# Kernel tuning notes

Measured on AMD Instinct MI355X. Metric: run time of the kernel, lower is better.

The kernel has to match this reference:

```python
import jax, jax.numpy as jnp
import numpy as np

NUM_HEADS = 6

def setup_inputs() -> dict:
    key = jax.random.key(0)
    k1, k2, k3 = jax.random.split(key, 3)
    B, N, C = 8, 4096, 768
    x = jax.random.normal(k1, (B, N, C), dtype=jnp.float32)
    # torch Linear weights, stored here as (in, out) so y = x @ w
    w_qkv = jax.random.normal(k2, (C, 3 * C), dtype=jnp.float32) * (C ** -0.5)
    w_proj = jax.random.normal(k3, (C, C), dtype=jnp.float32) * (C ** -0.5)
    b_proj = jnp.zeros((C,), dtype=jnp.float32)
    return {"x": x, "w_qkv": w_qkv, "w_proj": w_proj, "b_proj": b_proj}

def reference(x, w_qkv, w_proj, b_proj):
    B, N, C = x.shape
    H = NUM_HEADS
    D = C // H
    scale = D ** -0.5
    qkv = (x @ w_qkv).reshape(B, N, 3, H, D)
    q, k, v = qkv[:, :, 0], qkv[:, :, 1], qkv[:, :, 2]  # each (B, N, H, D)
    # NOTE: faithful to source — no permute, so attention is over the HEAD axis
    attn = jnp.einsum('bnhd,bngd->bnhg', q, k) * scale  # (B, N, H, H)
    attn = jax.nn.softmax(attn, axis=-1)
    out = jnp.einsum('bnhg,bngd->bnhd', attn, v)        # (B, N, H, D)
    # torch: .transpose(1,2).reshape(B, N, C) — replicate the exact dim mixing
    out = jnp.transpose(out, (0, 2, 1, 3)).reshape(B, N, C)
    return out @ w_proj + b_proj
```

## Files before the change

### kernel.cpp

```cpp
#include <hip/hip_runtime.h>
#include <hip/hip_bf16.h>
#include <stdint.h>

typedef __attribute__((ext_vector_type(8))) short short8;
typedef __attribute__((ext_vector_type(4))) float floatx4;

#define DEVINL static __device__ __forceinline__

DEVINL float bfu(short v) {
  union { uint32_t i; float f; } x; x.i = ((uint32_t)(uint16_t)v) << 16; return x.f;
}
DEVINL uint16_t f2bf(float f) {
  union { float f; uint32_t i; } x; x.f = f;
  uint32_t i = x.i;
  i += 0x7fff + ((i >> 16) & 1);
  return (uint16_t)(i >> 16);
}

DEVINL void transpose_tile(const float* in, uint16_t* out, int K, int N,
                           int bx, int by, float (*tile)[65]) {
  const int tn = bx * 64;
  const int tk = by * 64;
  const int tx = threadIdx.x & 63;
  const int ty = threadIdx.x >> 6;
#pragma unroll
  for (int i = 0; i < 64; i += 4)
    tile[ty + i][tx] = in[(long)(tk + ty + i) * N + tn + tx];
  __syncthreads();
#pragma unroll
  for (int i = 0; i < 64; i += 4)
    out[(long)(tn + ty + i) * K + tk + tx] = f2bf(tile[tx][ty + i]);
}

__global__ __launch_bounds__(256)
void k_prep(const float* __restrict__ x, uint16_t* __restrict__ x_bf, int n4,
            const float* __restrict__ w_qkv, uint16_t* __restrict__ wqkvT,
            const float* __restrict__ w_proj, uint16_t* __restrict__ wprojT) {
  __shared__ float tile[64][65];
  const int bid = blockIdx.x;
  if (bid < 2048) {
    int i = bid * 256 + threadIdx.x;
    const int stride = 2048 * 256;
    for (; i < n4; i += stride) {
      float4 v = ((const float4*)x)[i];
      ushort4 o;
      o.x = f2bf(v.x); o.y = f2bf(v.y); o.z = f2bf(v.z); o.w = f2bf(v.w);
      ((ushort4*)x_bf)[i] = o;
    }
  } else if (bid < 2048 + 36 * 12) {
    const int tq = bid - 2048;
    transpose_tile(w_qkv, wqkvT, 768, 2304, tq % 36, tq / 36, tile);
  } else {
    const int tp = bid - (2048 + 36 * 12);
    transpose_tile(w_proj, wprojT, 768, 768, tp % 12, tp / 12, tile);
  }
}

template<int OUT_BF16>
__global__ __launch_bounds__(256, 2)
void k_gemm128(const uint16_t* __restrict__ A,
               const uint16_t* __restrict__ B,
               void* __restrict__ Cout,
               const float* __restrict__ bias,
               int M, int N, int Kd, int tilesN)
{
  __shared__ uint16_t As[2][2][4096];
  __shared__ uint16_t Bs[2][2][4096];

  const int nwg = gridDim.x;
  const int orig = blockIdx.x;
  const int q = nwg >> 3, r = nwg & 7;
  const int xcd = orig & 7, seq = orig >> 3;
  const int wgid = (xcd < r ? xcd * (q + 1) : r * (q + 1) + (xcd - r) * q) + seq;
  const int mt = wgid / tilesN;
  const int nt = wgid - mt * tilesN;

  const int t = threadIdx.x;
  const int l = t & 63;
  const int w = t >> 6;
  const int wm = w >> 1;
  const int wn = w & 1;
  const long m0 = (long)mt * 128;
  const long n0 = (long)nt * 128;

  const int srow0 = t >> 3;
  const int scol  = ((l & 7) ^ (l >> 3)) * 8;
  const int wbyte = w * 1024;

  const uint16_t* Abase = A + m0 * Kd;
  const uint16_t* Bbase = B + n0 * Kd;

  const int fr = l & 15;
  const int kg = l >> 4;
  const int xorv = (l & 7) << 4;
  const int cb0 = (kg * 16) ^ xorv;
  const int cb1 = (64 + kg * 16) ^ xorv;

  floatx4 acc[4][4];
#pragma unroll
  for (int m = 0; m < 4; ++m)
#pragma unroll
    for (int n = 0; n < 4; ++n)
      acc[m][n] = (floatx4){0.f, 0.f, 0.f, 0.f};

  const int nK = Kd >> 6;

  auto stage = [&](uint16_t* ldsHalf, const uint16_t* gHalf, int ktile) {
    const uint16_t* g0 = gHalf + (long)srow0 * Kd + ktile * 64 + scol;
    __builtin_amdgcn_global_load_lds(
        (const __attribute__((address_space(1))) void*)g0,
        (__attribute__((address_space(3))) void*)((char*)ldsHalf + wbyte), 16, 0, 0);
    __builtin_amdgcn_global_load_lds(
        (const __attribute__((address_space(1))) void*)(g0 + (long)32 * Kd),
        (__attribute__((address_space(3))) void*)((char*)ldsHalf + 4096 + wbyte), 16, 0, 0);
  };
  auto rdA = [&](int buf, int mm, int kk) -> short8 {
    const char* p = (const char*)&As[buf][wm][0] + mm * 2048 + fr * 128 + (kk ? cb1 : cb0);
    return *(const short8*)p;
  };
  auto rdB = [&](int buf, int nn, int kk) -> short8 {
    const char* p = (const char*)&Bs[buf][wn][0] + nn * 2048 + fr * 128 + (kk ? cb1 : cb0);
    return *(const short8*)p;
  };

  stage(&Bs[0][0][0], Bbase, 0);
  stage(&Bs[0][1][0], Bbase + (long)64 * Kd, 0);
  stage(&As[0][0][0], Abase, 0);
  stage(&As[0][1][0], Abase + (long)64 * Kd, 0);
  {
    int t1 = 1 % nK;
    stage(&Bs[t1 & 1][0][0], Bbase, t1);
    stage(&As[t1 & 1][0][0], Abase, t1);
  }
  asm volatile("s_waitcnt vmcnt(4)" ::: "memory");
  __builtin_amdgcn_s_barrier();

  short8 a[4][2], bv0[2][2], bv1[2][2];

  for (int kt = 0; kt < nK; ++kt) {
    const int cbuf = kt & 1;
    const int nbuf = cbuf ^ 1;
    const int t1 = (kt + 1) % nK;
    const int t2 = (kt + 2) % nK;

#pragma unroll
    for (int mm = 0; mm < 4; ++mm) { a[mm][0] = rdA(cbuf, mm, 0); a[mm][1] = rdA(cbuf, mm, 1); }
#pragma unroll
    for (int nn = 0; nn < 2; ++nn) { bv0[nn][0] = rdB(cbuf, nn, 0); bv0[nn][1] = rdB(cbuf, nn, 1); }
#pragma unroll
    for (int nn = 0; nn < 2; ++nn) { bv1[nn][0] = rdB(cbuf, 2 + nn, 0); bv1[nn][1] = rdB(cbuf, 2 + nn, 1); }

    stage(&Bs[nbuf][1][0], Bbase + (long)64 * Kd, t1);
    stage(&As[nbuf][1][0], Abase + (long)64 * Kd, t1);

    asm volatile("s_waitcnt lgkmcnt(4)" ::: "memory");
    __builtin_amdgcn_s_setprio(1);
#pragma unroll
    for (int mm = 0; mm < 4; ++mm)
#pragma unroll
      for (int nn = 0; nn < 2; ++nn) {
        acc[mm][nn] = __builtin_amdgcn_mfma_f32_16x16x32_bf16(a[mm][0], bv0[nn][0], acc[mm][nn], 0, 0, 0);
        acc[mm][nn] = __builtin_amdgcn_mfma_f32_16x16x32_bf16(a[mm][1], bv0[nn][1], acc[mm][nn], 0, 0, 0);
      }
    asm volatile("s_waitcnt lgkmcnt(0)" ::: "memory");
    __builtin_amdgcn_s_barrier();

    stage(&Bs[cbuf][0][0], Bbase, t2);
    stage(&As[cbuf][0][0], Abase, t2);
#pragma unroll
    for (int mm = 0; mm < 4; ++mm)
#pragma unroll
      for (int nn = 0; nn < 2; ++nn) {
        acc[mm][2 + nn] = __builtin_amdgcn_mfma_f32_16x16x32_bf16(a[mm][0], bv1[nn][0], acc[mm][2 + nn], 0, 0, 0);
        acc[mm][2 + nn] = __builtin_amdgcn_mfma_f32_16x16x32_bf16(a[mm][1], bv1[nn][1], acc[mm][2 + nn], 0, 0, 0);
      }
    __builtin_amdgcn_s_setprio(0);

    asm volatile("s_waitcnt vmcnt(4)" ::: "memory");
    __builtin_amdgcn_s_barrier();
  }

  asm volatile("s_waitcnt vmcnt(0)" ::: "memory");
  __builtin_amdgcn_s_barrier();

  const int orow = (l >> 4) * 4;
  const int ocol = l & 15;
  if (OUT_BF16) {
    uint16_t* C = (uint16_t*)Cout;
    char* eb = (char*)&As[0][0][0] + (size_t)w * 4096;
    const int rr0 = l >> 3;
    const int cc0 = (l & 7) * 8;
#pragma unroll
    for (int mm = 0; mm < 4; ++mm) {
#pragma unroll
      for (int nn = 0; nn < 4; ++nn)
#pragma unroll
        for (int r2 = 0; r2 < 4; ++r2) {
          int rrow = orow + r2;
          int byo = ((rrow * 64 + nn * 16 + ocol) * 2) ^ ((rrow & 7) << 4);
          *(uint16_t*)(eb + byo) = f2bf(acc[mm][nn][r2]);
        }
#pragma unroll
      for (int p = 0; p < 2; ++p) {
        int rrow = rr0 + p * 8;
        int byo = ((rrow * 64 + cc0) * 2) ^ ((rrow & 7) << 4);
        short8 vvv = *(const short8*)(eb + byo);
        *(short8*)(&C[(m0 + wm * 64 + mm * 16 + rrow) * N + n0 + wn * 64 + cc0]) = vvv;
      }
    }
  } else {
    float* C = (float*)Cout;
    float* eb = (float*)&As[0][0][0] + (size_t)w * 1024;
    const int rr0 = l >> 4;
    const int cc0 = (l & 15) * 4;
    float4 bias4 = make_float4(0.f, 0.f, 0.f, 0.f);
    if (bias) bias4 = *(const float4*)(bias + n0 + wn * 64 + cc0);
#pragma unroll
    for (int mm = 0; mm < 4; ++mm) {
#pragma unroll
      for (int nn = 0; nn < 4; ++nn)
#pragma unroll
        for (int r2 = 0; r2 < 4; ++r2)
          eb[(orow + r2) * 64 + nn * 16 + ocol] = acc[mm][nn][r2];
#pragma unroll
      for (int p = 0; p < 4; ++p) {
        int rrow = rr0 + p * 4;
        float4 vvv = *(const float4*)(eb + rrow * 64 + cc0);
        vvv.x += bias4.x; vvv.y += bias4.y; vvv.z += bias4.z; vvv.w += bias4.w;
        *(float4*)(&C[(m0 + wm * 64 + mm * 16 + rrow) * N + n0 + wn * 64 + cc0]) = vvv;
      }
    }
  }
}

__global__ __launch_bounds__(256)
void k_attn(const uint16_t* __restrict__ qkv, uint16_t* __restrict__ outp) {
  const int wid = blockIdx.x * 4 + (threadIdx.x >> 6);
  const int l = threadIdx.x & 63;
  const int sub = l >> 4;
  const int i = l & 15;
  const int token = wid * 4 + sub;
  const uint16_t* row = qkv + (long)token * 2304 + i * 8;

  short8 kv[6];
  float qf[6][8];
#pragma unroll
  for (int h = 0; h < 6; ++h) {
    short8 qv = *(const short8*)(row + h * 128);
    kv[h] = *(const short8*)(row + 768 + h * 128);
#pragma unroll
    for (int e = 0; e < 8; ++e) qf[h][e] = bfu(qv[e]);
  }

  float s[36];
#pragma unroll
  for (int g = 0; g < 6; ++g) {
    float kf[8];
#pragma unroll
    for (int e = 0; e < 8; ++e) kf[e] = bfu(kv[g][e]);
#pragma unroll
    for (int h = 0; h < 6; ++h) {
      float a = 0.f;
#pragma unroll
      for (int e = 0; e < 8; ++e) a += qf[h][e] * kf[e];
      s[h * 6 + g] = a;
    }
  }

#pragma unroll
  for (int off = 8; off > 0; off >>= 1)
#pragma unroll
    for (int j = 0; j < 36; ++j)
      s[j] += __shfl_xor(s[j], off, 64);

  const float scale = 0.088388347648318447f;
  float p[36];
#pragma unroll
  for (int h = 0; h < 6; ++h) {
    float mx = s[h * 6];
#pragma unroll
    for (int g = 1; g < 6; ++g) mx = fmaxf(mx, s[h * 6 + g]);
    float sum = 0.f;
#pragma unroll
    for (int g = 0; g < 6; ++g) {
      float e = __expf((s[h * 6 + g] - mx) * scale);
      p[h * 6 + g] = e; sum += e;
    }
    float inv = 1.f / sum;
#pragma unroll
    for (int g = 0; g < 6; ++g) p[h * 6 + g] *= inv;
  }

  float o[6][8];
#pragma unroll
  for (int h = 0; h < 6; ++h)
#pragma unroll
    for (int e = 0; e < 8; ++e) o[h][e] = 0.f;
#pragma unroll
  for (int g = 0; g < 6; ++g) {
    short8 vv = *(const short8*)(row + 1536 + g * 128);
    float vf[8];
#pragma unroll
    for (int e = 0; e < 8; ++e) vf[e] = bfu(vv[e]);
#pragma unroll
    for (int h = 0; h < 6; ++h)
#pragma unroll
      for (int e = 0; e < 8; ++e) o[h][e] += p[h * 6 + g] * vf[e];
  }

  const int b = token >> 12, nn = token & 4095;
#pragma unroll
  for (int h = 0; h < 6; ++h) {
    short8 ov;
#pragma unroll
    for (int e = 0; e < 8; ++e) ov[e] = (short)f2bf(o[h][e]);
    *(short8*)(outp + ((long)(b * 6 + h) * 4096 + nn) * 128 + i * 8) = ov;
  }
}

extern "C" void kernel_launch(void* const* d_in, const int* in_sizes, int n_in,
                              void* d_out, int out_size, void* d_ws, size_t ws_size,
                              hipStream_t stream) {
  const float* x      = (const float*)d_in[0];
  const float* w_qkv  = (const float*)d_in[1];
  const float* w_proj = (const float*)d_in[2];
  const float* b_proj = (const float*)d_in[3];
  float* out = (float*)d_out;

  const int Cc = 768, C3 = 2304;
  const int Mtok = in_sizes[0] / Cc;

  char* ws = (char*)d_ws;
  uint16_t* x_bf   = (uint16_t*)ws;
  uint16_t* att_bf = x_bf;
  uint16_t* qkv_bf = (uint16_t*)(ws + 50331648);
  uint16_t* wqkvT  = (uint16_t*)(ws + 50331648 + 150994944);
  uint16_t* wprojT = (uint16_t*)(ws + 50331648 + 150994944 + 3538944);

  hipLaunchKernelGGL(k_prep, dim3(2048 + 432 + 144), dim3(256), 0, stream,
                     x, x_bf, Mtok * Cc / 4, w_qkv, wqkvT, w_proj, wprojT);

  hipLaunchKernelGGL((k_gemm128<1>), dim3((Mtok / 128) * (C3 / 128)), dim3(256), 0, stream,
                     x_bf, wqkvT, (void*)qkv_bf, (const float*)nullptr, Mtok, C3, Cc, C3 / 128);

  hipLaunchKernelGGL(k_attn, dim3(Mtok / 16), dim3(256), 0, stream, qkv_bf, att_bf);

  hipLaunchKernelGGL((k_gemm128<0>), dim3((Mtok / 128) * (Cc / 128)), dim3(256), 0, stream,
                     att_bf, wprojT, (void*)out, b_proj, Mtok, Cc, Cc, Cc / 128);
}
```

Baseline: 243.9 us.

## Add QKV GEMM variant loading B operand directly to registers

Adds a specialized QKV projection GEMM that stages only the A tile through LDS via global_load_lds, while each lane loads its B fragments straight from global memory into registers and double-buffers them. It also adds an epilogue that writes bf16 output through swizzled LDS so global stores are coalesced. The aim is to halve LDS traffic and shared memory use, and to overlap the next tile's loads with MFMA work. In exchange it issues more scattered global loads for B and uses more registers.

```diff
diff --git a/kernel.cpp b/kernel.cpp
--- a/kernel.cpp
+++ b/kernel.cpp
@@ -16,6 +16,7 @@
   i += 0x7fff + ((i >> 16) & 1);
   return (uint16_t)(i >> 16);
 }
+DEVINL short8 u4s8(uint4 v) { union { uint4 u; short8 s; } x; x.u = v; return x.s; }
 
 DEVINL void transpose_tile(const float* in, uint16_t* out, int K, int N,
                            int bx, int by, float (*tile)[65]) {
@@ -56,6 +57,159 @@
   }
 }
 
+__global__ __launch_bounds__(256, 2)
+void k_gemm1b(const uint16_t* __restrict__ A,
+              const uint16_t* __restrict__ B,
+              uint16_t* __restrict__ Cout,
+              int M, int N, int Kd, int tilesN)
+{
+  __shared__ uint16_t As[2][2][4096];
+
+  const int nwg = gridDim.x;
+  const int orig = blockIdx.x;
+  const int q = nwg >> 3, r = nwg & 7;
+  const int xcd = orig & 7, seq = orig >> 3;
+  const int wgid = (xcd < r ? xcd * (q + 1) : r * (q + 1) + (xcd - r) * q) + seq;
+  const int mt = wgid / tilesN;
+  const int nt = wgid - mt * tilesN;
+
+  const int t = threadIdx.x;
+  const int l = t & 63;
+  const int w = t >> 6;
+  const int wm = w >> 1;
+  const int wn = w & 1;
+  const long m0 = (long)mt * 128;
+  const long n0 = (long)nt * 128;
+
+  const int srow0 = t >> 3;
+  const int scol  = ((l & 7) ^ (l >> 3)) * 8;
+  const int wbyte = w * 1024;
+
+  const uint16_t* Abase = A + m0 * Kd;
+
+  const int fr = l & 15;
+  const int kg = l >> 4;
+  const int xorv = (l & 7) << 4;
+  const int cb0 = (kg * 16) ^ xorv;
+  const int cb1 = (64 + kg * 16) ^ xorv;
+
+  const uint16_t* Blane = B + (n0 + wn * 64 + fr) * Kd + kg * 8;
+
+  floatx4 acc[4][4];
+#pragma unroll
+  for (int m = 0; m < 4; ++m)
+#pragma unroll
+    for (int n = 0; n < 4; ++n)
+      acc[m][n] = (floatx4){0.f, 0.f, 0.f, 0.f};
+
+  const int nK = Kd >> 6;
+
+  auto stage = [&](uint16_t* ldsHalf, const uint16_t* gHalf, int ktile) {
+    const uint16_t* g0 = gHalf + (long)srow0 * Kd + ktile * 64 + scol;
+    __builtin_amdgcn_global_load_lds(
+        (const __attribute__((address_space(1))) void*)g0,
+        (__attribute__((address_space(3))) void*)((char*)ldsHalf + wbyte), 16, 0, 0);
+    __builtin_amdgcn_global_load_lds(
+        (const __attribute__((address_space(1))) void*)(g0 + (long)32 * Kd),
+        (__attribute__((address_space(3))) void*)((char*)ldsHalf + 4096 + wbyte), 16, 0, 0);
+  };
+  auto rdA = [&](int buf, int mm, int kk) -> short8 {
+    const char* p = (const char*)&As[buf][wm][0] + mm * 2048 + fr * 128 + (kk ? cb1 : cb0);
+    return *(const short8*)p;
+  };
+
+  short8 a[4][2];
+  uint4 bp[8], bq[8];
+
+#define LOADB(DST, KT) do {                                                  \
+    const uint16_t* gB_ = Blane + (long)(KT) * 64;                           \
+    _Pragma("unroll")                                                        \
+    for (int nn_ = 0; nn_ < 4; ++nn_) {                                      \
+      DST[nn_ * 2]     = *(const uint4*)(gB_ + (long)nn_ * 16 * Kd);         \
+      DST[nn_ * 2 + 1] = *(const uint4*)(gB_ + (long)nn_ * 16 * Kd + 32);    \
+    }                                                                        \
+  } while (0)
+
+#define TILE(CBUF, KT, BU, BL) do {                                          \
+    const int t1_ = ((KT) + 1) % nK;                                         \
+    const int t2_ = ((KT) + 2) % nK;                                         \
+    _Pragma("unroll")                                                        \
+    for (int mm_ = 0; mm_ < 4; ++mm_) {                                      \
+      a[mm_][0] = rdA(CBUF, mm_, 0); a[mm_][1] = rdA(CBUF, mm_, 1);          \
+    }                                                                        \
+    stage(&As[(CBUF) ^ 1][1][0], Abase + (long)64 * Kd, t1_);                \
+    LOADB(BL, t1_);                                                          \
+    asm volatile("s_waitcnt lgkmcnt(0)" ::: "memory");                       \
+    __builtin_amdgcn_s_setprio(1);                                          \
+    _Pragma("unroll")                                                        \
+    for (int mm_ = 0; mm_ < 4; ++mm_)                                        \
+      _Pragma("unroll")                                                      \
+      for (int nn_ = 0; nn_ < 2; ++nn_) {                                    \
+        acc[mm_][nn_] = __builtin_amdgcn_mfma_f32_16x16x32_bf16(             \
+            a[mm_][0], u4s8(BU[nn_ * 2]), acc[mm_][nn_], 0, 0, 0);           \
+        acc[mm_][nn_] = __builtin_amdgcn_mfma_f32_16x16x32_bf16(             \
+            a[mm_][1], u4s8(BU[nn_ * 2 + 1]), acc[mm_][nn_], 0, 0, 0);       \
+      }                                                                      \
+    __builtin_amdgcn_s_barrier();                                           \
+    stage(&As[CBUF][0][0], Abase, t2_);                                      \
+    _Pragma("unroll")                                                        \
+    for (int mm_ = 0; mm_ < 4; ++mm_)                                        \
+      _Pragma("unroll")                                                      \
+      for (int nn_ = 0; nn_ < 2; ++nn_) {                                    \
+        acc[mm_][2 + nn_] = __builtin_amdgcn_mfma_f32_16x16x32_bf16(         \
+            a[mm_][0], u4s8(BU[(2 + nn_) * 2]), acc[mm_][2 + nn_], 0, 0, 0); \
+        acc[mm_][2 + nn_] = __builtin_amdgcn_mfma_f32_16x16x32_bf16(         \
+            a[mm_][1], u4s8(BU[(2 + nn_) * 2 + 1]), acc[mm_][2 + nn_], 0, 0, 0); \
+      }                                                                      \
+    __builtin_amdgcn_s_setprio(0);                                          \
+    asm volatile("s_waitcnt vmcnt(2)" ::: "memory");                         \
+    __builtin_amdgcn_s_barrier();                                           \
+  } while (0)
+
+  stage(&As[0][0][0], Abase, 0);
+  stage(&As[0][1][0], Abase + (long)64 * Kd, 0);
+  LOADB(bp, 0);
+  stage(&As[1][0][0], Abase, 1 % nK);
+  asm volatile("s_waitcnt vmcnt(2)" ::: "memory");
+  __builtin_amdgcn_s_barrier();
+
+  for (int kt2 = 0; kt2 < nK; kt2 += 2) {
+    TILE(0, kt2, bp, bq);
+    TILE(1, kt2 + 1, bq, bp);
+  }
+#undef TILE
+#undef LOADB
+
+  asm volatile("s_waitcnt vmcnt(0)" ::: "memory");
+  __builtin_amdgcn_s_barrier();
+
+  const int orow = (l >> 4) * 4;
+  const int ocol = l & 15;
+  {
+    char* eb = (char*)&As[0][0][0] + (size_t)w * 4096;
+    const int rr0 = l >> 3;
+    const int cc0 = (l & 7) * 8;
+#pragma unroll
+    for (int mm = 0; mm < 4; ++mm) {
+#pragma unroll
+      for (int nn = 0; nn < 4; ++nn)
+#pragma unroll
+        for (int r2 = 0; r2 < 4; ++r2) {
+          int rrow = orow + r2;
+          int byo = ((rrow * 64 + nn * 16 + ocol) * 2) ^ ((rrow & 7) << 4);
+          *(uint16_t*)(eb + byo) = f2bf(acc[mm][nn][r2]);
+        }
+#pragma unroll
+      for (int p = 0; p < 2; ++p) {
+        int rrow = rr0 + p * 8;
+        int byo = ((rrow * 64 + cc0) * 2) ^ ((rrow & 7) << 4);
+        short8 vvv = *(const short8*)(eb + byo);
+        *(short8*)(&Cout[(m0 + wm * 64 + mm * 16 + rrow) * N + n0 + wn * 64 + cc0]) = vvv;
+      }
+    }
+  }
+}
+
 template<int OUT_BF16>
 __global__ __launch_bounds__(256, 2)
 void k_gemm128(const uint16_t* __restrict__ A,
@@ -340,8 +494,8 @@
   hipLaunchKernelGGL(k_prep, dim3(2048 + 432 + 144), dim3(256), 0, stream,
                      x, x_bf, Mtok * Cc / 4, w_qkv, wqkvT, w_proj, wprojT);
 
-  hipLaunchKernelGGL((k_gemm128<1>), dim3((Mtok / 128) * (C3 / 128)), dim3(256), 0, stream,
-                     x_bf, wqkvT, (void*)qkv_bf, (const float*)nullptr, Mtok, C3, Cc, C3 / 128);
+  hipLaunchKernelGGL(k_gemm1b, dim3((Mtok / 128) * (C3 / 128)), dim3(256), 0, stream,
+                     x_bf, wqkvT, qkv_bf, Mtok, C3, Cc, C3 / 128);
 
   hipLaunchKernelGGL(k_attn, dim3(Mtok / 16), dim3(256), 0, stream, qkv_bf, att_bf);
 
```

New measurement: 388.4 us. 59.2% more time.
